# Optimization experiments

Hardware: AMD Instinct MI355X
Metric: run time of the kernel (lower is better)

## Reference

```python
import jax, jax.numpy as jnp
import numpy as np

N_NODES = 100000
N_EDGES = 3200000
IN_FEATS = 256
OUT_FEATS = 128
N_LAYERS = 3


def setup_inputs() -> dict:
    key = jax.random.key(0)
    k1, k2, k3, k4, k5, k6 = jax.random.split(key, 6)
    x = jax.random.normal(k1, (N_NODES, IN_FEATS), dtype=jnp.float32)
    row = jax.random.randint(k2, (N_EDGES,), 0, N_NODES, dtype=jnp.int64)
    col = jax.random.randint(k3, (N_EDGES,), 0, N_NODES, dtype=jnp.int64)
    vals = jax.random.uniform(k4, (N_EDGES,), dtype=jnp.float32)
    W = jax.random.normal(k5, (OUT_FEATS, IN_FEATS), dtype=jnp.float32) * (1.0 / np.sqrt(IN_FEATS))
    b = jax.random.normal(k6, (OUT_FEATS,), dtype=jnp.float32) * 0.01
    return {"x": x, "row": row, "col": col, "vals": vals, "W": W, "b": b, "n_layers": N_LAYERS}


def reference(x, row, col, vals, W, b, n_layers):
    n_nodes = x.shape[0]
    # z = linear(x)
    z = jnp.einsum('ni,oi->no', x, W) + b  # [N, out_feats]
    # repeated SpMM: z_new[r] = sum over edges e with row[e]==r of vals[e] * z[col[e]]
    for _ in range(int(n_layers)):
        gathered = vals[:, None] * z[col]  # [E, out_feats]
        z = jax.ops.segment_sum(gathered, row, num_segments=n_nodes)
    return z
```

## Files before the change

kernel.cpp:

```cpp
#include <hip/hip_runtime.h>
#include <hip/hip_bf16.h>

#define NNODES   100000
#define INF      256
#define OUTF     128
#define NLAYERS  3

#define RPB   196
#define NBKT  511
#define CAP   7168
#define EPB   8192

typedef unsigned short u16;

typedef __attribute__((ext_vector_type(8))) __bf16 bf16x8;
typedef __attribute__((ext_vector_type(4))) float  f32x4;

__device__ __forceinline__ float bf2f(u16 u) {
    union { unsigned int i; float f; } c; c.i = ((unsigned int)u) << 16; return c.f;
}
__device__ __forceinline__ u16 f2bf(float f) {
    union { float f; unsigned int i; } c; c.f = f;
    unsigned int lsb = (c.i >> 16) & 1;
    return (u16)((c.i + 0x7FFF + lsb) >> 16);
}

__global__ __launch_bounds__(256) void wconv_kernel(const float* __restrict__ W,
                                                    u16* __restrict__ Wbf) {
    int i = (blockIdx.x * 256 + threadIdx.x) * 4;
    float4 a = *(const float4*)(W + i);
    ushort4 o;
    o.x = f2bf(a.x); o.y = f2bf(a.y); o.z = f2bf(a.z); o.w = f2bf(a.w);
    *(ushort4*)(Wbf + i) = o;
}

__global__ __launch_bounds__(256) void partition_kernel(
    const int* __restrict__ row, const int* __restrict__ col,
    const float* __restrict__ vals, int* __restrict__ alloc,
    int2* __restrict__ epart, int E)
{
    __shared__ int hist[NBKT];
    __shared__ int gbase[NBKT];
    int tid = threadIdx.x;
    int e0  = blockIdx.x * EPB;

    for (int i = tid; i < NBKT; i += 256) hist[i] = 0;
    __syncthreads();
    for (int i = tid * 4; i < EPB; i += 1024) {
        int e = e0 + i;
        if (e < E) {
            int4 r4 = *(const int4*)(row + e);
            atomicAdd(&hist[r4.x / RPB], 1);
            atomicAdd(&hist[r4.y / RPB], 1);
            atomicAdd(&hist[r4.z / RPB], 1);
            atomicAdd(&hist[r4.w / RPB], 1);
        }
    }
    __syncthreads();
    for (int i = tid; i < NBKT; i += 256) {
        int c = hist[i];
        gbase[i] = c ? atomicAdd(&alloc[i], c) : 0;
    }
    __syncthreads();
    for (int i = tid; i < NBKT; i += 256) hist[i] = 0;
    __syncthreads();
    for (int i = tid * 4; i < EPB; i += 1024) {
        int e = e0 + i;
        if (e < E) {
            int4   r4 = *(const int4*)(row + e);
            int4   c4 = *(const int4*)(col + e);
            float4 v4 = *(const float4*)(vals + e);
            int   rr[4] = {r4.x, r4.y, r4.z, r4.w};
            int   cc[4] = {c4.x, c4.y, c4.z, c4.w};
            float vv[4] = {v4.x, v4.y, v4.z, v4.w};
#pragma unroll
            for (int t = 0; t < 4; ++t) {
                int b    = rr[t] / RPB;
                int lofs = atomicAdd(&hist[b], 1);
                epart[(size_t)b * CAP + gbase[b] + lofs] =
                    make_int2(cc[t] | ((rr[t] - b * RPB) << 17), __float_as_int(vv[t]));
            }
        }
    }
}

__global__ __launch_bounds__(256) void bucket_scatter_kernel(
    const int* __restrict__ alloc, int2* __restrict__ epart,
    int* __restrict__ rowptr, int* __restrict__ rowcnt, int M)
{
    int b = blockIdx.x;
    int n = alloc[b];
    int2* src = epart + (size_t)b * CAP;
    __shared__ int2 stage[CAP];
    __shared__ int  hist[256];
    __shared__ int  excl[256];
    __shared__ int  wofs[RPB];
    int tid = threadIdx.x;

    for (int i = tid; i < n; i += 256) stage[i] = src[i];
    hist[tid] = 0;
    __syncthreads();
    for (int i = tid; i < n; i += 256) atomicAdd(&hist[stage[i].x >> 17], 1);
    __syncthreads();
    int v = hist[tid];
    int w = (v + 1) & ~1;
    excl[tid] = w;
    __syncthreads();
    for (int off = 1; off < 256; off <<= 1) {
        int t = (tid >= off) ? excl[tid - off] : 0;
        __syncthreads();
        excl[tid] += t;
        __syncthreads();
    }
    int ex = excl[tid] - w;
    int r  = b * RPB + tid;
    if (tid < RPB && r < M) {
        rowptr[r] = b * CAP + ex;
        rowcnt[r] = v;
    }
    if (tid < RPB) wofs[tid] = ex;
    __syncthreads();
    for (int i = tid; i < n; i += 256) {
        int2 p  = stage[i];
        int  rl = p.x >> 17;
        int  pos = atomicAdd(&wofs[rl], 1);
        src[pos] = make_int2(p.x & 0x1FFFF, p.y);
    }
}

__global__ __launch_bounds__(256) void gemm_mfma_kernel(
    const float* __restrict__ x, const u16* __restrict__ Wbf,
    const float* __restrict__ b, u16* __restrict__ z, int M, int ntiles)
{
    __shared__ __align__(16) u16 Wl[128 * 256];
    int tid  = threadIdx.x;
    int lane = tid & 63;
    int wv   = tid >> 6;

    {
        int c = tid >> 1;
        int h = tid & 1;
        const bf16x8* src = (const bf16x8*)(Wbf + c * 256 + h * 128);
        u16* dst = Wl + c * 256;
        int swz = c & 7;
#pragma unroll
        for (int t = 0; t < 16; ++t) {
            int j = h * 16 + t;
            *(bf16x8*)(dst + 8 * (j ^ swz)) = src[t];
        }
    }

    int cl = lane & 15;
    int g  = lane >> 4;
    float bo[8];
#pragma unroll
    for (int f = 0; f < 8; ++f) bo[f] = b[16 * f + cl];

    __syncthreads();

    for (int tile = blockIdx.x; tile < ntiles; tile += gridDim.x) {
        int n0 = tile * 64 + wv * 16;
        int nr = n0 + cl;
        if (nr >= M) nr = M - 1;
        const float* xrow = x + (size_t)nr * INF + 8 * g;

        f32x4 acc[8];
#pragma unroll
        for (int f = 0; f < 8; ++f) {
            f32x4 a; a[0] = bo[f]; a[1] = bo[f]; a[2] = bo[f]; a[3] = bo[f];
            acc[f] = a;
        }

#pragma unroll
        for (int ks = 0; ks < 8; ++ks) {
            int k0 = ks * 32;
            float4 a0 = ((const float4*)(xrow + k0))[0];
            float4 a1 = ((const float4*)(xrow + k0))[1];
            bf16x8 af;
            af[0] = (__bf16)a0.x; af[1] = (__bf16)a0.y;
            af[2] = (__bf16)a0.z; af[3] = (__bf16)a0.w;
            af[4] = (__bf16)a1.x; af[5] = (__bf16)a1.y;
            af[6] = (__bf16)a1.z; af[7] = (__bf16)a1.w;
#pragma unroll
            for (int f = 0; f < 8; ++f) {
                int c  = 16 * f + cl;
                int ke = (k0 + 8 * g) ^ ((c & 7) << 3);
                bf16x8 bfr = *(const bf16x8*)(Wl + c * 256 + ke);
                acc[f] = __builtin_amdgcn_mfma_f32_16x16x32_bf16(af, bfr, acc[f], 0, 0, 0);
            }
        }

        int rbase = n0 + 4 * g;
#pragma unroll
        for (int j = 0; j < 4; ++j) {
            int n = rbase + j;
            if (n < M) {
                u16* zr = z + (size_t)n * OUTF;
#pragma unroll
                for (int f = 0; f < 8; ++f)
                    zr[16 * f + cl] = f2bf(acc[f][j]);
            }
        }
    }
}

template <bool MASKED>
__device__ __forceinline__ void edge8(const int2* __restrict__ ep, int e, int end,
                                      const u16* __restrict__ zin, int f,
                                      float2* __restrict__ acc) {
    int2 p[8];
#pragma unroll
    for (int i = 0; i < 8; ++i) {
        int idx = MASKED ? ((e + i < end) ? e + i : end - 1) : (e + i);
        p[i] = ep[idx];
    }
    ushort2 zb[8];
#pragma unroll
    for (int i = 0; i < 8; ++i)
        zb[i] = *(const ushort2*)(zin + (size_t)p[i].x * OUTF + f);
#pragma unroll
    for (int i = 0; i < 8; ++i) {
        float v = __int_as_float(p[i].y);
        if (MASKED) v = (e + i < end) ? v : 0.f;
        acc[i & 3].x += v * bf2f(zb[i].x);
        acc[i & 3].y += v * bf2f(zb[i].y);
    }
}

template <bool OUT_BF16>
__global__ __launch_bounds__(256) void spmm_kernel(const int* __restrict__ rowptr,
                                                   const int* __restrict__ rowcnt,
                                                   const int2* __restrict__ epart,
                                                   const u16* __restrict__ zin,
                                                   void* __restrict__ zout, int M) {
    int r = blockIdx.x * 4 + (threadIdx.x >> 6);
    if (r >= M) return;
    int lane = threadIdx.x & 63;
    int f    = lane * 2;

    int start = __builtin_amdgcn_readfirstlane(rowptr[r]);
    int n     = __builtin_amdgcn_readfirstlane(rowcnt[r]);
    int end   = start + n;

    float2 acc[4] = {{0.f,0.f},{0.f,0.f},{0.f,0.f},{0.f,0.f}};
    int e = start;
    for (; e + 16 <= end; e += 16) {
        int4 q[8];
#pragma unroll
        for (int j = 0; j < 8; ++j) q[j] = *((const int4*)(epart + e) + j);
        __builtin_amdgcn_sched_barrier(0);
        ushort2 zb[16];
#pragma unroll
        for (int j = 0; j < 8; ++j) {
            zb[2*j]   = *(const ushort2*)(zin + (size_t)q[j].x * OUTF + f);
            zb[2*j+1] = *(const ushort2*)(zin + (size_t)q[j].z * OUTF + f);
        }
        __builtin_amdgcn_sched_barrier(0);
#pragma unroll
        for (int j = 0; j < 8; ++j) {
            float v0 = __int_as_float(q[j].y);
            float v1 = __int_as_float(q[j].w);
            acc[(2*j)   & 3].x += v0 * bf2f(zb[2*j].x);
            acc[(2*j)   & 3].y += v0 * bf2f(zb[2*j].y);
            acc[(2*j+1) & 3].x += v1 * bf2f(zb[2*j+1].x);
            acc[(2*j+1) & 3].y += v1 * bf2f(zb[2*j+1].y);
        }
    }
    for (; e < end; e += 8) edge8<true>(epart, e, end, zin, f, acc);

    float sx = (acc[0].x + acc[1].x) + (acc[2].x + acc[3].x);
    float sy = (acc[0].y + acc[1].y) + (acc[2].y + acc[3].y);
    if (OUT_BF16) {
        ushort2 o; o.x = f2bf(sx); o.y = f2bf(sy);
        *(ushort2*)((u16*)zout + (size_t)r * OUTF + f) = o;
    } else {
        *(float2*)((float*)zout + (size_t)r * OUTF + f) = make_float2(sx, sy);
    }
}


extern "C" void kernel_launch(void* const* d_in, const int* in_sizes, int n_in,
                              void* d_out, int out_size, void* d_ws, size_t ws_size,
                              hipStream_t stream) {
    const float* x    = (const float*)d_in[0];
    const int*   row  = (const int*)d_in[1];
    const int*   col  = (const int*)d_in[2];
    const float* vals = (const float*)d_in[3];
    const float* W    = (const float*)d_in[4];
    const float* b    = (const float*)d_in[5];
    float* out = (float*)d_out;

    const int M = in_sizes[0] / INF;
    const int E = in_sizes[1];

    u16*   zb0    = (u16*)d_ws;
    u16*   zb1    = zb0 + (size_t)M * OUTF;
    int*   rowptr = (int*)(zb1 + (size_t)M * OUTF);
    int*   rowcnt = rowptr + M;
    int*   alloc  = rowcnt + M;
    size_t wb_ofs = (size_t)((char*)(alloc + NBKT) - (char*)d_ws);
    wb_ofs = (wb_ofs + 15) & ~(size_t)15;
    u16*   Wbf    = (u16*)((char*)d_ws + wb_ofs);
    size_t ep_ofs = wb_ofs + (size_t)OUTF * INF * sizeof(u16);
    ep_ofs = (ep_ofs + 15) & ~(size_t)15;
    int2*  epart  = (int2*)((char*)d_ws + ep_ofs);

    wconv_kernel<<<(OUTF * INF) / 1024, 256, 0, stream>>>(W, Wbf);

    hipMemsetAsync(alloc, 0, NBKT * sizeof(int), stream);
    partition_kernel<<<(E + EPB - 1) / EPB, 256, 0, stream>>>(row, col, vals, alloc, epart, E);
    bucket_scatter_kernel<<<NBKT, 256, 0, stream>>>(alloc, epart, rowptr, rowcnt, M);

    int ntiles = (M + 63) / 64;
    gemm_mfma_kernel<<<512, 256, 0, stream>>>(x, Wbf, b, zb0, M, ntiles);

    int sgrid = (M + 3) / 4;
    spmm_kernel<true ><<<sgrid, 256, 0, stream>>>(rowptr, rowcnt, epart, zb0, (void*)zb1, M);
    spmm_kernel<true ><<<sgrid, 256, 0, stream>>>(rowptr, rowcnt, epart, zb1, (void*)zb0, M);
    spmm_kernel<false><<<sgrid, 256, 0, stream>>>(rowptr, rowcnt, epart, zb0, (void*)out, M);
}
```

Measured before the change: 610.2 us.

## Replace global atomic bucket allocation with per-block offset table and gather pass

The partition kernel no longer reserves space with global atomics per bucket. Each block now writes its edges, locally bucket-sorted, into a private chunk and records per-bucket offsets in a table. The bucket kernel then scans that table column to gather each bucket's segments from all blocks before the row-level sort. The output is deterministic and avoids contended global atomics and the memset, but it adds a second edge buffer and many small, uncoalesced serial per-thread copies in the gather.

```diff
diff --git a/kernel.cpp b/kernel.cpp
--- a/kernel.cpp
+++ b/kernel.cpp
@@ -9,7 +9,8 @@
 #define RPB   196
 #define NBKT  511
 #define CAP   7168
-#define EPB   8192
+#define EPB   4096
+#define NBLKMAX 1024
 
 typedef unsigned short u16;
 
@@ -36,75 +37,124 @@
 
 __global__ __launch_bounds__(256) void partition_kernel(
     const int* __restrict__ row, const int* __restrict__ col,
-    const float* __restrict__ vals, int* __restrict__ alloc,
-    int2* __restrict__ epart, int E)
+    const float* __restrict__ vals, int2* __restrict__ epart1,
+    int* __restrict__ table, int E)
 {
     __shared__ int hist[NBKT];
-    __shared__ int gbase[NBKT];
+    __shared__ int base[NBKT];
+    __shared__ int part[256];
     int tid = threadIdx.x;
-    int e0  = blockIdx.x * EPB;
+    int blk = blockIdx.x;
+    int e0  = blk * EPB;
+    int nE  = E - e0; if (nE > EPB) nE = EPB;
 
     for (int i = tid; i < NBKT; i += 256) hist[i] = 0;
     __syncthreads();
-    for (int i = tid * 4; i < EPB; i += 1024) {
+    for (int i = tid * 4; i < nE; i += 1024) {
+        int4 r4 = *(const int4*)(row + e0 + i);
+        atomicAdd(&hist[r4.x / RPB], 1);
+        atomicAdd(&hist[r4.y / RPB], 1);
+        atomicAdd(&hist[r4.z / RPB], 1);
+        atomicAdd(&hist[r4.w / RPB], 1);
+    }
+    __syncthreads();
+    int i0 = tid * 4;
+    int w[4]; int s = 0;
+#pragma unroll
+    for (int k = 0; k < 4; ++k) {
+        int v = (i0 + k < NBKT) ? hist[i0 + k] : 0;
+        w[k] = s; s += v;
+    }
+    part[tid] = s;
+    __syncthreads();
+    for (int off = 1; off < 256; off <<= 1) {
+        int t = (tid >= off) ? part[tid - off] : 0;
+        __syncthreads();
+        part[tid] += t;
+        __syncthreads();
+    }
+    int bex = part[tid] - s;
+#pragma unroll
+    for (int k = 0; k < 4; ++k) {
+        if (i0 + k < NBKT) {
+            int o = bex + w[k];
+            base[i0 + k] = o;
+            table[(size_t)blk * NBKT + i0 + k] = o;
+        }
+    }
+    __syncthreads();
+    for (int i = tid; i < NBKT; i += 256) hist[i] = 0;
+    __syncthreads();
+    int2* dst = epart1 + (size_t)blk * EPB;
+    for (int i = tid * 4; i < nE; i += 1024) {
         int e = e0 + i;
-        if (e < E) {
-            int4 r4 = *(const int4*)(row + e);
-            atomicAdd(&hist[r4.x / RPB], 1);
-            atomicAdd(&hist[r4.y / RPB], 1);
-            atomicAdd(&hist[r4.z / RPB], 1);
-            atomicAdd(&hist[r4.w / RPB], 1);
-        }
-    }
-    __syncthreads();
-    for (int i = tid; i < NBKT; i += 256) {
-        int c = hist[i];
-        gbase[i] = c ? atomicAdd(&alloc[i], c) : 0;
-    }
-    __syncthreads();
-    for (int i = tid; i < NBKT; i += 256) hist[i] = 0;
-    __syncthreads();
-    for (int i = tid * 4; i < EPB; i += 1024) {
-        int e = e0 + i;
-        if (e < E) {
-            int4   r4 = *(const int4*)(row + e);
-            int4   c4 = *(const int4*)(col + e);
-            float4 v4 = *(const float4*)(vals + e);
-            int   rr[4] = {r4.x, r4.y, r4.z, r4.w};
-            int   cc[4] = {c4.x, c4.y, c4.z, c4.w};
-            float vv[4] = {v4.x, v4.y, v4.z, v4.w};
-#pragma unroll
-            for (int t = 0; t < 4; ++t) {
-                int b    = rr[t] / RPB;
-                int lofs = atomicAdd(&hist[b], 1);
-                epart[(size_t)b * CAP + gbase[b] + lofs] =
-                    make_int2(cc[t] | ((rr[t] - b * RPB) << 17), __float_as_int(vv[t]));
-            }
-        }
-    }
-}
-
-__global__ __launch_bounds__(256) void bucket_scatter_kernel(
-    const int* __restrict__ alloc, int2* __restrict__ epart,
-    int* __restrict__ rowptr, int* __restrict__ rowcnt, int M)
+        int4   r4 = *(const int4*)(row + e);
+        int4   c4 = *(const int4*)(col + e);
+        float4 v4 = *(const float4*)(vals + e);
+        int   rr[4] = {r4.x, r4.y, r4.z, r4.w};
+        int   cc[4] = {c4.x, c4.y, c4.z, c4.w};
+        float vv[4] = {v4.x, v4.y, v4.z, v4.w};
+#pragma unroll
+        for (int t = 0; t < 4; ++t) {
+            int b    = rr[t] / RPB;
+            int lofs = atomicAdd(&hist[b], 1);
+            dst[base[b] + lofs] =
+                make_int2(cc[t] | ((rr[t] - b * RPB) << 17), __float_as_int(vv[t]));
+        }
+    }
+}
+
+__global__ __launch_bounds__(256) void bucket_gather_kernel(
+    const int* __restrict__ table, const int2* __restrict__ epart1,
+    int2* __restrict__ epart2, int* __restrict__ rowptr,
+    int* __restrict__ rowcnt, int M, int E, int nblk)
 {
-    int b = blockIdx.x;
-    int n = alloc[b];
-    int2* src = epart + (size_t)b * CAP;
+    int b   = blockIdx.x;
+    int tid = threadIdx.x;
     __shared__ int2 stage[CAP];
+    __shared__ int  part[256];
     __shared__ int  hist[256];
     __shared__ int  excl[256];
     __shared__ int  wofs[RPB];
-    int tid = threadIdx.x;
-
-    for (int i = tid; i < n; i += 256) stage[i] = src[i];
+
+    int fo[4], fl[4], fw[4]; int s = 0;
+#pragma unroll
+    for (int k = 0; k < 4; ++k) {
+        int blk = tid * 4 + k;
+        fo[k] = 0; fl[k] = 0;
+        if (blk < nblk) {
+            int o  = table[(size_t)blk * NBKT + b];
+            int nE = E - blk * EPB; if (nE > EPB) nE = EPB;
+            int oN = (b + 1 < NBKT) ? table[(size_t)blk * NBKT + b + 1] : nE;
+            fo[k] = o; fl[k] = oN - o;
+        }
+        fw[k] = s; s += fl[k];
+    }
+    part[tid] = s;
+    __syncthreads();
+    for (int off = 1; off < 256; off <<= 1) {
+        int t = (tid >= off) ? part[tid - off] : 0;
+        __syncthreads();
+        part[tid] += t;
+        __syncthreads();
+    }
+    int bex = part[tid] - s;
+    int n   = part[255];
+#pragma unroll
+    for (int k = 0; k < 4; ++k) {
+        if (fl[k] > 0) {
+            const int2* sp = epart1 + (size_t)(tid * 4 + k) * EPB + fo[k];
+            int d = bex + fw[k];
+            for (int j = 0; j < fl[k]; ++j) stage[d + j] = sp[j];
+        }
+    }
     hist[tid] = 0;
     __syncthreads();
     for (int i = tid; i < n; i += 256) atomicAdd(&hist[stage[i].x >> 17], 1);
     __syncthreads();
     int v = hist[tid];
-    int w = (v + 1) & ~1;
-    excl[tid] = w;
+    int wpad = (v + 1) & ~1;
+    excl[tid] = wpad;
     __syncthreads();
     for (int off = 1; off < 256; off <<= 1) {
         int t = (tid >= off) ? excl[tid - off] : 0;
@@ -112,7 +162,7 @@
         excl[tid] += t;
         __syncthreads();
     }
-    int ex = excl[tid] - w;
+    int ex = excl[tid] - wpad;
     int r  = b * RPB + tid;
     if (tid < RPB && r < M) {
         rowptr[r] = b * CAP + ex;
@@ -120,11 +170,12 @@
     }
     if (tid < RPB) wofs[tid] = ex;
     __syncthreads();
+    int2* dst = epart2 + (size_t)b * CAP;
     for (int i = tid; i < n; i += 256) {
         int2 p  = stage[i];
         int  rl = p.x >> 17;
         int  pos = atomicAdd(&wofs[rl], 1);
-        src[pos] = make_int2(p.x & 0x1FFFF, p.y);
+        dst[pos] = make_int2(p.x & 0x1FFFF, p.y);
     }
 }
 
@@ -292,30 +343,33 @@
 
     const int M = in_sizes[0] / INF;
     const int E = in_sizes[1];
+    const int nblk = (E + EPB - 1) / EPB;
 
     u16*   zb0    = (u16*)d_ws;
     u16*   zb1    = zb0 + (size_t)M * OUTF;
     int*   rowptr = (int*)(zb1 + (size_t)M * OUTF);
     int*   rowcnt = rowptr + M;
-    int*   alloc  = rowcnt + M;
-    size_t wb_ofs = (size_t)((char*)(alloc + NBKT) - (char*)d_ws);
+    int*   table  = rowcnt + M;
+    size_t wb_ofs = (size_t)((char*)(table + (size_t)NBLKMAX * NBKT) - (char*)d_ws);
     wb_ofs = (wb_ofs + 15) & ~(size_t)15;
     u16*   Wbf    = (u16*)((char*)d_ws + wb_ofs);
-    size_t ep_ofs = wb_ofs + (size_t)OUTF * INF * sizeof(u16);
-    ep_ofs = (ep_ofs + 15) & ~(size_t)15;
-    int2*  epart  = (int2*)((char*)d_ws + ep_ofs);
+    size_t e1_ofs = wb_ofs + (size_t)OUTF * INF * sizeof(u16);
+    e1_ofs = (e1_ofs + 15) & ~(size_t)15;
+    int2*  epart1 = (int2*)((char*)d_ws + e1_ofs);
+    size_t e2_ofs = e1_ofs + (size_t)NBLKMAX * EPB * sizeof(int2);
+    int2*  epart2 = (int2*)((char*)d_ws + e2_ofs);
 
     wconv_kernel<<<(OUTF * INF) / 1024, 256, 0, stream>>>(W, Wbf);
 
-    hipMemsetAsync(alloc, 0, NBKT * sizeof(int), stream);
-    partition_kernel<<<(E + EPB - 1) / EPB, 256, 0, stream>>>(row, col, vals, alloc, epart, E);
-    bucket_scatter_kernel<<<NBKT, 256, 0, stream>>>(alloc, epart, rowptr, rowcnt, M);
+    partition_kernel<<<nblk, 256, 0, stream>>>(row, col, vals, epart1, table, E);
+    bucket_gather_kernel<<<NBKT, 256, 0, stream>>>(table, epart1, epart2,
+                                                   rowptr, rowcnt, M, E, nblk);
 
     int ntiles = (M + 63) / 64;
     gemm_mfma_kernel<<<512, 256, 0, stream>>>(x, Wbf, b, zb0, M, ntiles);
 
     int sgrid = (M + 3) / 4;
-    spmm_kernel<true ><<<sgrid, 256, 0, stream>>>(rowptr, rowcnt, epart, zb0, (void*)zb1, M);
-    spmm_kernel<true ><<<sgrid, 256, 0, stream>>>(rowptr, rowcnt, epart, zb1, (void*)zb0, M);
-    spmm_kernel<false><<<sgrid, 256, 0, stream>>>(rowptr, rowcnt, epart, zb0, (void*)out, M);
-}
+    spmm_kernel<true ><<<sgrid, 256, 0, stream>>>(rowptr, rowcnt, epart2, zb0, (void*)zb1, M);
+    spmm_kernel<true ><<<sgrid, 256, 0, stream>>>(rowptr, rowcnt, epart2, zb1, (void*)zb0, M);
+    spmm_kernel<false><<<sgrid, 256, 0, stream>>>(rowptr, rowcnt, epart2, zb0, (void*)out, M);
+}
```

New measurement: 598.7 us. Within noise of the previous version (-1.9%).
